# Optimization experiments

Hardware: AMD Instinct MI355X
Metric: run time of the kernel (lower is better)

Reference implementation:

```python
import jax, jax.numpy as jnp
import numpy as np

QMIN, QMAX = 0.0, 255.0  # uint8 export range

def _round_half_away(x):
    # torch _round_nearest_without_round: round half away from zero
    return jnp.where(x < 0, -jnp.floor(-x + 0.5), jnp.floor(x + 0.5))

def setup_inputs() -> dict:
    key = jax.random.key(0)
    k = jax.random.split(key, 7)
    B, S, DIN, DOUT = 2, 2048, 2048, 8192
    x = jax.random.normal(k[0], (B, S, DIN), dtype=jnp.float32)
    # per-tensor activation qparams (keep scale away from 0)
    a_scale = jax.random.uniform(k[1], (1,), dtype=jnp.float32) * 0.05 + 0.01
    a_zp = jax.random.randint(k[2], (1,), 100, 156, dtype=jnp.int32)
    # pre-quantized uint8 weight stored as int32, per-out-channel qparams
    weight_q = jax.random.randint(k[3], (DOUT, DIN), 0, 256, dtype=jnp.int32)
    w_scale = jax.random.uniform(k[4], (DOUT,), dtype=jnp.float32) * 0.02 + 0.001
    w_zp = jax.random.randint(k[5], (DOUT,), 100, 156, dtype=jnp.int32)
    bias = jax.random.normal(k[6], (DOUT,), dtype=jnp.float32)
    return {"x": x, "a_scale": a_scale, "a_zp": a_zp, "weight_q": weight_q,
            "w_scale": w_scale, "w_zp": w_zp, "bias": bias}

def reference(x, a_scale, a_zp, weight_q, w_scale, w_zp, bias):
    dt = x.dtype
    # --- activation fake-quant (ExportAffineQuantizer, per-tensor) ---
    s = a_scale.astype(dt).reshape((1,) * x.ndim)
    z = a_zp.astype(dt).reshape((1,) * x.ndim)
    x_q = jnp.clip(_round_half_away(x / s) + z, QMIN, QMAX)
    x_dq = (x_q - z) * s
    # --- weight dequant (ExportWeightBackedLinear, ch_axis=0) ---
    # W: [out, in] = (w_q - zp) * scale, broadcast over in-dim
    W = (weight_q.astype(dt) - w_zp.astype(dt)[:, None]) * w_scale.astype(dt)[:, None]
    # --- linear: [B,S,in] @ [in,out] + bias ---
    return jnp.einsum('bsk,ok->bso', x_dq, W) + bias.astype(dt)
```

## Files before the change

### kernel.cpp

```cpp
#include <hip/hip_runtime.h>
#include <hip/hip_bf16.h>

#define M_DIM 4096
#define K_DIM 2048
#define N_DIM 8192

#define NT 32

typedef int   int32x4  __attribute__((ext_vector_type(4)));
typedef int   int32x16 __attribute__((ext_vector_type(16)));

#define XC_OFF 0
#define WC_OFF 8388608UL
#define RX_OFF 25165824UL
#define AL_OFF 25182208UL
#define G_OFF  25214976UL
#define F0_OFF 25247744UL

__device__ __forceinline__ int pack4(int a, int b, int c, int d) {
    return (a & 255) | ((b & 255) << 8) | ((c & 255) << 16) | ((d & 255) << 24);
}

__global__ __launch_bounds__(256) void prep_x_kernel(
    const float4* __restrict__ x, signed char* __restrict__ xc, int* __restrict__ rx,
    const float* __restrict__ a_scale, const int* __restrict__ a_zp)
{
    const int row = blockIdx.x;
    const int tid = threadIdx.x;
    const float s = a_scale[0];
    const float z = (float)a_zp[0];
    int sum = 0;
    int* xci = (int*)(xc + (size_t)row * K_DIM);
    const float4* xr = x + (size_t)row * (K_DIM / 4);
    #pragma unroll
    for (int it = 0; it < 2; ++it) {
        int qi = tid + it * 256;
        float4 v = xr[qi];
        int q0 = (int)(fminf(fmaxf(roundf(v.x / s) + z, 0.f), 255.f)) - 128;
        int q1 = (int)(fminf(fmaxf(roundf(v.y / s) + z, 0.f), 255.f)) - 128;
        int q2 = (int)(fminf(fmaxf(roundf(v.z / s) + z, 0.f), 255.f)) - 128;
        int q3 = (int)(fminf(fmaxf(roundf(v.w / s) + z, 0.f), 255.f)) - 128;
        sum += q0 + q1 + q2 + q3;
        xci[qi] = pack4(q0, q1, q2, q3);
    }
    #pragma unroll
    for (int off = 32; off > 0; off >>= 1) sum += __shfl_down(sum, off);
    __shared__ int wsum[4];
    if ((tid & 63) == 0) wsum[tid >> 6] = sum;
    __syncthreads();
    if (tid == 0) rx[row] = wsum[0] + wsum[1] + wsum[2] + wsum[3];
}

__global__ __launch_bounds__(256) void prep_w_kernel(
    const int4* __restrict__ wq, signed char* __restrict__ wc,
    int* __restrict__ al, float* __restrict__ g, float* __restrict__ F0,
    const float* __restrict__ a_scale, const int* __restrict__ a_zp,
    const float* __restrict__ w_scale, const int* __restrict__ w_zp,
    const float* __restrict__ bias)
{
    const int o   = blockIdx.x;
    const int tid = threadIdx.x;
    int sum = 0;
    int* wci = (int*)(wc + (size_t)o * K_DIM);
    const int4* wr = wq + (size_t)o * (K_DIM / 4);
    #pragma unroll
    for (int it = 0; it < 2; ++it) {
        int qi = tid + it * 256;
        int4 v = wr[qi];
        int q0 = v.x - 128, q1 = v.y - 128, q2 = v.z - 128, q3 = v.w - 128;
        sum += q0 + q1 + q2 + q3;
        wci[qi] = pack4(q0, q1, q2, q3);
    }
    #pragma unroll
    for (int off = 32; off > 0; off >>= 1) sum += __shfl_down(sum, off);
    __shared__ int wsum[4];
    if ((tid & 63) == 0) wsum[tid >> 6] = sum;
    __syncthreads();
    if (tid == 0) {
        int rw    = wsum[0] + wsum[1] + wsum[2] + wsum[3];
        int alpha = 128 - w_zp[o];
        int beta  = 128 - a_zp[0];
        int C0    = beta * (rw + K_DIM * alpha);
        float gg  = a_scale[0] * w_scale[o];
        al[o] = alpha;
        g[o]  = gg;
        F0[o] = gg * (float)C0 + bias[o];
    }
}


__device__ __forceinline__ void glds16(const void* gptr, void* lptr) {
    __builtin_amdgcn_global_load_lds(
        (const __attribute__((address_space(1))) void*)gptr,
        (__attribute__((address_space(3))) void*)lptr, 16, 0, 0);
}

__global__ __launch_bounds__(512) void gemm_i8_kernel(
    const signed char* __restrict__ A,
    const signed char* __restrict__ Bw,
    const int*   __restrict__ rx,
    const int*   __restrict__ al,
    const float* __restrict__ g,
    const float* __restrict__ F0,
    float* __restrict__ C)
{
    extern __shared__ signed char lds[];
    signed char* ldsA = lds;
    signed char* ldsB = lds + 65536;

    const int tid  = threadIdx.x;
    const int lane = tid & 63;
    const int wave = tid >> 6;
    const int wr   = wave >> 2;
    const int wc   = wave & 3;
    const int l31  = lane & 31;
    const int lk   = lane >> 5;
    const int rsw  = (l31 >> 1) & 3;

    const int bid = blockIdx.x;
    const int swz = (bid & 7) * 64 + (bid >> 3);
    const int bn0 = (swz & 31) * 256;
    const int bm0 = (swz >> 5) * 256;

    const int  sr  = tid >> 2;
    const int  spc = (tid & 3) ^ ((sr >> 1) & 3);
    const signed char* srcA0 = A  + (size_t)(bm0 + sr) * K_DIM + spc * 16;
    const signed char* srcA1 = srcA0 + (size_t)128 * K_DIM;
    const signed char* srcB0 = Bw + (size_t)(bn0 + sr) * K_DIM + spc * 16;
    const signed char* srcB1 = srcB0 + (size_t)128 * K_DIM;
    signed char* dstA0 = ldsA + tid * 16;
    signed char* dstB0 = ldsB + tid * 16;

#define STAGE_A(s) { const int kof = (s) * 64; const int bo = ((s) & 3) * 16384; \
    glds16(srcA0 + kof, dstA0 + bo); glds16(srcA1 + kof, dstA0 + bo + 8192); }
#define STAGE_B(s) { const int kof = (s) * 64; const int bo = ((s) & 3) * 16384; \
    glds16(srcB0 + kof, dstB0 + bo); glds16(srcB1 + kof, dstB0 + bo + 8192); }

    int arowb[4], browb[2];
    #pragma unroll
    for (int im = 0; im < 4; ++im) arowb[im] = (wr * 128 + im * 32 + l31) * 64;
    #pragma unroll
    for (int jn = 0; jn < 2; ++jn) browb[jn] = (wc * 64 + jn * 32 + l31) * 64;
    const int aoff0 = ((0 + lk) ^ rsw) << 4;
    const int aoff1 = ((2 + lk) ^ rsw) << 4;

    int32x16 acc[4][2];
    #pragma unroll
    for (int im = 0; im < 4; ++im)
        #pragma unroll
        for (int jn = 0; jn < 2; ++jn)
            acc[im][jn] = (int32x16)(0);

#define TILE_PH(T, AOFF, STAGE_STMT) { \
    const int bo_ = ((T) & 3) * 16384; \
    int32x4 af[4], bf[2]; \
    _Pragma("unroll") for (int im = 0; im < 4; ++im) \
        af[im] = *(const int32x4*)(ldsA + bo_ + arowb[im] + (AOFF)); \
    _Pragma("unroll") for (int jn = 0; jn < 2; ++jn) \
        bf[jn] = *(const int32x4*)(ldsB + bo_ + browb[jn] + (AOFF)); \
    STAGE_STMT; \
    __builtin_amdgcn_s_barrier(); \
    __builtin_amdgcn_s_setprio(1); \
    _Pragma("unroll") for (int im = 0; im < 4; ++im) \
        _Pragma("unroll") for (int jn = 0; jn < 2; ++jn) \
            acc[im][jn] = __builtin_amdgcn_mfma_i32_32x32x32_i8(af[im], bf[jn], acc[im][jn], 0, 0, 0); \
    __builtin_amdgcn_s_setprio(0); \
}

#define MIDBAR __builtin_amdgcn_s_barrier();
#define BOUND(N) { asm volatile("s_waitcnt vmcnt(" #N ")" ::: "memory"); __builtin_amdgcn_s_barrier(); }

    STAGE_A(0); STAGE_B(0);
    STAGE_A(1); STAGE_B(1);
    STAGE_A(2); STAGE_B(2);
    asm volatile("s_waitcnt vmcnt(8)" ::: "memory");
    __builtin_amdgcn_s_barrier();

    #pragma unroll 1
    for (int t = 0; t < 29; ++t) {
        TILE_PH(t, aoff0, STAGE_A(t + 3)); MIDBAR;
        TILE_PH(t, aoff1, STAGE_B(t + 3));
        BOUND(8);
    }
    TILE_PH(29, aoff0, ((void)0)); MIDBAR;
    TILE_PH(29, aoff1, ((void)0)); BOUND(4);
    TILE_PH(30, aoff0, ((void)0)); MIDBAR;
    TILE_PH(30, aoff1, ((void)0)); BOUND(0);
    TILE_PH(31, aoff0, ((void)0)); MIDBAR;
    TILE_PH(31, aoff1, ((void)0));

    #pragma unroll
    for (int im = 0; im < 4; ++im) {
        int rxv[16];
        #pragma unroll
        for (int r = 0; r < 16; ++r)
            rxv[r] = rx[bm0 + wr * 128 + im * 32 + (r & 3) + 8 * (r >> 2) + 4 * lk];
        #pragma unroll
        for (int jn = 0; jn < 2; ++jn) {
            const int col = bn0 + wc * 64 + jn * 32 + l31;
            const float gg = g[col];
            const float ff = F0[col];
            const int   aa = al[col];
            #pragma unroll
            for (int r = 0; r < 16; ++r) {
                const int grow = bm0 + wr * 128 + im * 32 + (r & 3) + 8 * (r >> 2) + 4 * lk;
                const int tv = acc[im][jn][r] + aa * rxv[r];
                C[(size_t)grow * N_DIM + col] = fmaf(gg, (float)tv, ff);
            }
        }
    }
#undef TILE_PH
#undef STAGE_A
#undef STAGE_B
#undef MIDBAR
#undef BOUND
}


extern "C" void kernel_launch(void* const* d_in, const int* in_sizes, int n_in,
                              void* d_out, int out_size, void* d_ws, size_t ws_size,
                              hipStream_t stream) {
    const float* x        = (const float*)d_in[0];
    const float* a_scale  = (const float*)d_in[1];
    const int*   a_zp     = (const int*)d_in[2];
    const int*   weight_q = (const int*)d_in[3];
    const float* w_scale  = (const float*)d_in[4];
    const int*   w_zp     = (const int*)d_in[5];
    const float* bias     = (const float*)d_in[6];
    float*       out      = (float*)d_out;

    char* ws = (char*)d_ws;
    signed char* xc = (signed char*)(ws + XC_OFF);
    signed char* wc = (signed char*)(ws + WC_OFF);
    int*   rx = (int*)(ws + RX_OFF);
    int*   al = (int*)(ws + AL_OFF);
    float* g  = (float*)(ws + G_OFF);
    float* F0 = (float*)(ws + F0_OFF);

    prep_x_kernel<<<M_DIM, 256, 0, stream>>>((const float4*)x, xc, rx, a_scale, a_zp);
    prep_w_kernel<<<N_DIM, 256, 0, stream>>>((const int4*)weight_q, wc, al, g, F0,
                                             a_scale, a_zp, w_scale, w_zp, bias);

    gemm_i8_kernel<<<512, 512, 131072, stream>>>(xc, wc, rx, al, g, F0, out);
}
```

Baseline: 292.1 us.

## Pack row pairs into 128-byte LDS lines with 8-way XOR swizzle, drop mid barriers

The GEMM's LDS staging layout changes from one 64-byte row per line with a 4-way swizzle to two adjacent rows packed into each 128-byte line. The 16-byte chunk index is XOR-swizzled over 8 positions, and the fragment read offsets are recomputed to match. The aim is to cut bank conflicts on the 128-bit LDS fragment reads. It also removes the extra barrier between the two half-K phases of each tile, since each phase already contains a barrier. Together these should lower LDS stall and synchronisation overhead in the main loop, at the cost of more complex address arithmetic.

New measurement: 288.9 us. Within noise of the previous version (-1.1%).

```diff
diff --git a/kernel.cpp b/kernel.cpp
--- a/kernel.cpp
+++ b/kernel.cpp
@@ -4,8 +4,6 @@
 #define M_DIM 4096
 #define K_DIM 2048
 #define N_DIM 8192
-
-#define NT 32
 
 typedef int   int32x4  __attribute__((ext_vector_type(4)));
 typedef int   int32x16 __attribute__((ext_vector_type(16)));
@@ -115,18 +113,19 @@
     const int wc   = wave & 3;
     const int l31  = lane & 31;
     const int lk   = lane >> 5;
-    const int rsw  = (l31 >> 1) & 3;
 
     const int bid = blockIdx.x;
     const int swz = (bid & 7) * 64 + (bid >> 3);
     const int bn0 = (swz & 31) * 256;
     const int bm0 = (swz >> 5) * 256;
 
-    const int  sr  = tid >> 2;
-    const int  spc = (tid & 3) ^ ((sr >> 1) & 3);
-    const signed char* srcA0 = A  + (size_t)(bm0 + sr) * K_DIM + spc * 16;
+    const int slr = tid >> 3;
+    const int cg  = (tid & 7) ^ (slr & 7);
+    const int sp  = cg >> 2;
+    const int skc = cg & 3;
+    const signed char* srcA0 = A  + (size_t)(bm0 + 2 * slr + sp) * K_DIM + skc * 16;
     const signed char* srcA1 = srcA0 + (size_t)128 * K_DIM;
-    const signed char* srcB0 = Bw + (size_t)(bn0 + sr) * K_DIM + spc * 16;
+    const signed char* srcB0 = Bw + (size_t)(bn0 + 2 * slr + sp) * K_DIM + skc * 16;
     const signed char* srcB1 = srcB0 + (size_t)128 * K_DIM;
     signed char* dstA0 = ldsA + tid * 16;
     signed char* dstB0 = ldsB + tid * 16;
@@ -136,13 +135,17 @@
 #define STAGE_B(s) { const int kof = (s) * 64; const int bo = ((s) & 3) * 16384; \
     glds16(srcB0 + kof, dstB0 + bo); glds16(srcB1 + kof, dstB0 + bo + 8192); }
 
+    const int q  = l31 >> 1;
+    const int e  = q & 7;
+    const int pp = l31 & 1;
     int arowb[4], browb[2];
     #pragma unroll
-    for (int im = 0; im < 4; ++im) arowb[im] = (wr * 128 + im * 32 + l31) * 64;
-    #pragma unroll
-    for (int jn = 0; jn < 2; ++jn) browb[jn] = (wc * 64 + jn * 32 + l31) * 64;
-    const int aoff0 = ((0 + lk) ^ rsw) << 4;
-    const int aoff1 = ((2 + lk) ^ rsw) << 4;
+    for (int im = 0; im < 4; ++im) arowb[im] = (wr * 64 + im * 16 + q) * 128;
+    #pragma unroll
+    for (int jn = 0; jn < 2; ++jn) browb[jn] = (wc * 32 + jn * 16 + q) * 128;
+    const int aoff0 = ((pp * 4 + lk) ^ e) * 16;
+    const int aoff1 = aoff0 ^ 32;
+    (void)aoff1;
 
     int32x16 acc[4][2];
     #pragma unroll
@@ -167,7 +170,6 @@
     __builtin_amdgcn_s_setprio(0); \
 }
 
-#define MIDBAR __builtin_amdgcn_s_barrier();
 #define BOUND(N) { asm volatile("s_waitcnt vmcnt(" #N ")" ::: "memory"); __builtin_amdgcn_s_barrier(); }
 
     STAGE_A(0); STAGE_B(0);
@@ -178,15 +180,15 @@
 
     #pragma unroll 1
     for (int t = 0; t < 29; ++t) {
-        TILE_PH(t, aoff0, STAGE_A(t + 3)); MIDBAR;
+        TILE_PH(t, aoff0, STAGE_A(t + 3));
         TILE_PH(t, aoff1, STAGE_B(t + 3));
         BOUND(8);
     }
-    TILE_PH(29, aoff0, ((void)0)); MIDBAR;
+    TILE_PH(29, aoff0, ((void)0));
     TILE_PH(29, aoff1, ((void)0)); BOUND(4);
-    TILE_PH(30, aoff0, ((void)0)); MIDBAR;
+    TILE_PH(30, aoff0, ((void)0));
     TILE_PH(30, aoff1, ((void)0)); BOUND(0);
-    TILE_PH(31, aoff0, ((void)0)); MIDBAR;
+    TILE_PH(31, aoff0, ((void)0));
     TILE_PH(31, aoff1, ((void)0));
 
     #pragma unroll
@@ -212,7 +214,6 @@
 #undef TILE_PH
 #undef STAGE_A
 #undef STAGE_B
-#undef MIDBAR
 #undef BOUND
 }
 
```
